# Performance work log

Hardware: AMD Instinct MI355X
Metric: run time of the kernel (lower is better)

The kernel has to match this reference:

```python
import jax, jax.numpy as jnp
import numpy as np

N, M, D, H = 16, 1024, 64, 4  # batch, num_node, dim_in==dim_hid, num_head
NEG_SLOPE = 0.2


def setup_inputs() -> dict:
    key = jax.random.key(0)
    ks = jax.random.split(key, 10)
    s = 1.0 / np.sqrt(D)
    inp = {
        "x": jax.random.normal(ks[0], (N, M, D), dtype=jnp.float32),
        "edge": jnp.zeros((N, M, M), dtype=jnp.float32),  # unused by the module
        # stacked per-head Linear(dim_in, dim_hid) params: weight (H, D_out, D_in), bias (H, D_out)
        "Wk": (jax.random.normal(ks[1], (H, D, D), dtype=jnp.float32) * s),
        "bk": (jax.random.normal(ks[2], (H, D), dtype=jnp.float32) * s),
        "Wq": (jax.random.normal(ks[3], (H, D, D), dtype=jnp.float32) * s),
        "bq": (jax.random.normal(ks[4], (H, D), dtype=jnp.float32) * s),
        "Wv": (jax.random.normal(ks[5], (H, D, D), dtype=jnp.float32) * s),
        "bv": (jax.random.normal(ks[6], (H, D), dtype=jnp.float32) * s),
        # decoder: Linear(dim_hid*num_head -> dim_in)
        "Wdec": (jax.random.normal(ks[7], (D, H * D), dtype=jnp.float32) / np.sqrt(H * D)),
        "bdec": (jax.random.normal(ks[8], (D,), dtype=jnp.float32) / np.sqrt(H * D)),
    }
    return inp


def reference(x, edge, Wk, bk, Wq, bq, Wv, bv, Wdec, bdec):
    # x: (N, M, D). Per head h: K = x @ Wk[h].T + bk[h], etc.
    K = jnp.einsum("nmd,hed->nhme", x, Wk) + bk[None, :, None, :]  # (N,H,M,D)
    Q = jnp.einsum("nmd,hed->nhme", x, Wq) + bq[None, :, None, :]
    V = jnp.einsum("nmd,hed->nhme", x, Wv) + bv[None, :, None, :]
    # alpha[n,h,i,j] = K[n,h,i] . Q[n,h,j]  (sender=K row i, receiver=Q row j)
    alpha = jnp.einsum("nhie,nhje->nhij", K, Q)  # (N,H,M,M)
    alpha = jax.nn.leaky_relu(alpha, NEG_SLOPE)
    alpha = jax.nn.softmax(alpha, axis=-1)
    agg = jnp.einsum("nhij,nhje->nhie", alpha, V)  # (N,H,M,D)
    dx = jax.nn.leaky_relu(agg, NEG_SLOPE) - x[:, None, :, :]  # (N,H,M,D)
    # concat heads along feature dim (head 0 first): (N, M, H*D)
    dx = dx.transpose(0, 2, 1, 3).reshape(N, M, H * D)
    return dx @ Wdec.T + bdec  # (N, M, D)
```

## Files before the change

### kernel.cpp

```cpp
#include <hip/hip_runtime.h>
#include <hip/hip_bf16.h>


#define NB 16
#define MM 1024
#define DD 64
#define HH 4
#define NEG 0.2f
#define AST 72
#define DST 264

typedef __attribute__((ext_vector_type(8))) short bf16x8;
typedef __attribute__((ext_vector_type(8))) _Float16 f16x8;
typedef __attribute__((ext_vector_type(16))) float f32x16;

__device__ inline unsigned short f2bf(float f) {
  unsigned int u = __builtin_bit_cast(unsigned int, f);
  return (unsigned short)((u + 0x7FFFu + ((u >> 16) & 1u)) >> 16);
}
__device__ inline unsigned short f2h(float f) {
  _Float16 h = (_Float16)f;
  return __builtin_bit_cast(unsigned short, h);
}
__device__ inline unsigned int pack_bf16(float a, float b) {
  unsigned int ua = __builtin_bit_cast(unsigned int, a);
  unsigned int ub = __builtin_bit_cast(unsigned int, b);
  ua = (ua + 0x7FFFu + ((ua >> 16) & 1u)) >> 16;
  ub = (ub + 0x7FFFu + ((ub >> 16) & 1u)) & 0xFFFF0000u;
  return ua | ub;
}

__global__ __launch_bounds__(256) void proj_kernel(
    const float* __restrict__ x,
    const float* __restrict__ Wk, const float* __restrict__ Wq, const float* __restrict__ Wv,
    const float* __restrict__ bk, const float* __restrict__ bq, const float* __restrict__ bv,
    unsigned short* __restrict__ Kf, unsigned short* __restrict__ Qf,
    unsigned short* __restrict__ Vtg) {
  __shared__ unsigned short xs[64 * AST];
  __shared__ unsigned short ob[64 * AST];
  const int t = threadIdx.x;
  const int r0 = blockIdx.x * 64;
  const int combo = blockIdx.y, mat = combo >> 2, h = combo & 3;
  const int n = r0 >> 10, ml = r0 & 1023;
  const float* W = mat == 0 ? Wk : (mat == 1 ? Wq : Wv);
  const float* bias = mat == 0 ? bk : (mat == 1 ? bq : bv);

#pragma unroll
  for (int rep = 0; rep < 2; ++rep) {
    int idx = rep * 256 + t, row = idx >> 3, c8 = (idx & 7) * 8;
    float4 a = *(const float4*)&x[(size_t)(r0 + row) * DD + c8];
    float4 b = *(const float4*)&x[(size_t)(r0 + row) * DD + c8 + 4];
    unsigned short p[8] = {f2h(a.x), f2h(a.y), f2h(a.z), f2h(a.w),
                           f2h(b.x), f2h(b.y), f2h(b.z), f2h(b.w)};
    *(uint4*)&xs[row * AST + c8] = *(uint4*)p;
  }
  __syncthreads();

  const int w = t >> 6, lane = t & 63, m31 = lane & 31, hf = lane >> 5;
  const int mi = w >> 1, ne = w & 1;
  const int ecol = h * 64 + ne * 32 + m31;
  const float bb = bias[ecol];

  f32x16 C;
#pragma unroll
  for (int r = 0; r < 16; ++r) C[r] = 0.f;
#pragma unroll
  for (int ks = 0; ks < 4; ++ks) {
    f16x8 xa = *(f16x8*)&xs[(mi * 32 + m31) * AST + ks * 16 + hf * 8];
    float4 wa = *(const float4*)&W[(size_t)ecol * DD + ks * 16 + hf * 8];
    float4 wc = *(const float4*)&W[(size_t)ecol * DD + ks * 16 + hf * 8 + 4];
    f16x8 wb;
    wb[0] = (_Float16)wa.x; wb[1] = (_Float16)wa.y; wb[2] = (_Float16)wa.z; wb[3] = (_Float16)wa.w;
    wb[4] = (_Float16)wc.x; wb[5] = (_Float16)wc.y; wb[6] = (_Float16)wc.z; wb[7] = (_Float16)wc.w;
    C = __builtin_amdgcn_mfma_f32_32x32x16_f16(xa, wb, C, 0, 0, 0);
  }

  if (mat < 2) {
#pragma unroll
    for (int r = 0; r < 16; ++r) {
      int rr = (r & 3) + 8 * (r >> 2) + 4 * hf;
      ob[(mi * 32 + rr) * AST + ne * 32 + m31] = f2h(C[r] + bb);
    }
  } else {
#pragma unroll
    for (int r = 0; r < 16; ++r) {
      int rr = (r & 3) + 8 * (r >> 2) + 4 * hf;
      ob[(ne * 32 + m31) * AST + mi * 32 + rr] = f2bf(C[r] + bb);
    }
  }
  __syncthreads();

  if (mat < 2) {
    unsigned short* dst = mat == 0 ? Kf : Qf;
    const size_t obase = (((size_t)n * HH + h) * MM + ml) * DD;
#pragma unroll
    for (int rep = 0; rep < 2; ++rep) {
      int idx = rep * 256 + t, row = idx >> 3, c8 = (idx & 7) * 8;
      *(uint4*)&dst[obase + (size_t)row * DD + c8] = *(uint4*)&ob[row * AST + c8];
    }
  } else {
    const size_t obase = (((size_t)n * HH + h) * DD) * MM + ml;
#pragma unroll
    for (int rep = 0; rep < 2; ++rep) {
      int idx = rep * 256 + t, row = idx >> 3, c8 = (idx & 7) * 8;
      *(uint4*)&Vtg[obase + (size_t)row * MM + c8] = *(uint4*)&ob[row * AST + c8];
    }
  }
}

__global__ __launch_bounds__(256, 4) void attn_kernel(
    const unsigned short* __restrict__ Kf, const unsigned short* __restrict__ Qf,
    const unsigned short* __restrict__ Vtg, const float* __restrict__ x,
    unsigned short* __restrict__ DX) {
  __shared__ unsigned short smem[2 * 64 * AST];
  __shared__ float lsp[2][64];
  unsigned short* qh = smem;
  unsigned short* vt = smem + 64 * AST;

  const int t = threadIdx.x;
  const int w = t >> 6, lane = t & 63, m31 = lane & 31, hf = lane >> 5;
  const int ih = w >> 1, jh = w & 1;
  const int i0 = blockIdx.x * 64, h = blockIdx.y, n = blockIdx.z;
  const size_t base = (((size_t)n * HH + h) * MM) * DD;
  const size_t baseT = (((size_t)n * HH + h) * DD) * MM;
  const int irow = i0 + ih * 32 + m31;

  f16x8 kf[4];
#pragma unroll
  for (int ks = 0; ks < 4; ++ks)
    kf[ks] = *(const f16x8*)&Kf[base + (size_t)irow * DD + ks * 16 + hf * 8];

  f32x16 agg0, agg1;
#pragma unroll
  for (int r = 0; r < 16; ++r) { agg0[r] = 0.f; agg1[r] = 0.f; }
  float lsum = 0.f;

  for (int jt = 0; jt < 16; ++jt) {
    const int j0 = jt * 64;
    __syncthreads();
#pragma unroll
    for (int rep = 0; rep < 2; ++rep) {
      int idx = rep * 256 + t, row = idx >> 3, c8 = (idx & 7) * 8;
      *(uint4*)&qh[row * AST + c8] = *(const uint4*)&Qf[base + (size_t)(j0 + row) * DD + c8];
      *(uint4*)&vt[row * AST + c8] = *(const uint4*)&Vtg[baseT + (size_t)row * MM + j0 + c8];
    }
    __syncthreads();

    f32x16 C;
#pragma unroll
    for (int r = 0; r < 16; ++r) C[r] = 0.f;
#pragma unroll
    for (int ks = 0; ks < 4; ++ks) {
      f16x8 qa = *(f16x8*)&qh[(jh * 32 + m31) * AST + ks * 16 + hf * 8];
      C = __builtin_amdgcn_mfma_f32_32x32x16_f16(qa, kf[ks], C, 0, 0, 0);
    }
    unsigned int pk[8];
#pragma unroll
    for (int g = 0; g < 4; ++g) {
      float p0 = C[4 * g + 0], p1 = C[4 * g + 1], p2 = C[4 * g + 2], p3 = C[4 * g + 3];
      p0 = __expf(fmaxf(p0, NEG * p0));
      p1 = __expf(fmaxf(p1, NEG * p1));
      p2 = __expf(fmaxf(p2, NEG * p2));
      p3 = __expf(fmaxf(p3, NEG * p3));
      lsum += (p0 + p1) + (p2 + p3);
      pk[g * 2]     = pack_bf16(p0, p1);
      pk[g * 2 + 1] = pack_bf16(p2, p3);
    }

#pragma unroll
    for (int kk = 0; kk < 2; ++kk) {
      const int gl2 = kk * 4, gh2 = kk * 4 + 2;
      unsigned int sA = hf ? pk[gl2]     : pk[gh2];
      unsigned int sB = hf ? pk[gl2 + 1] : pk[gh2 + 1];
      unsigned int rA = (unsigned int)__shfl_xor((int)sA, 32);
      unsigned int rB = (unsigned int)__shfl_xor((int)sB, 32);
      union { unsigned int u[4]; bf16x8 v; } cv;
      cv.u[0] = hf ? rA : pk[gl2];
      cv.u[1] = hf ? rB : pk[gl2 + 1];
      cv.u[2] = hf ? pk[gh2]     : rA;
      cv.u[3] = hf ? pk[gh2 + 1] : rB;
      bf16x8 bV0 = *(bf16x8*)&vt[m31 * AST + jh * 32 + kk * 16 + hf * 8];
      bf16x8 bV1 = *(bf16x8*)&vt[(32 + m31) * AST + jh * 32 + kk * 16 + hf * 8];
      agg0 = __builtin_amdgcn_mfma_f32_32x32x16_bf16(cv.v, bV0, agg0, 0, 0, 0);
      agg1 = __builtin_amdgcn_mfma_f32_32x32x16_bf16(cv.v, bV1, agg1, 0, 0, 0);
    }
  }

  lsum += __shfl_xor(lsum, 32);
  __syncthreads();
  if (hf == 0) lsp[jh][ih * 32 + m31] = lsum;
  float* red = (float*)smem;
  const int slot = ih * 2304 + m31 * 72 + hf * 36;
  if (jh == 1) {
#pragma unroll
    for (int c = 0; c < 4; ++c) {
      *(float4*)&red[slot + 4 * c]      = make_float4(agg0[4*c], agg0[4*c+1], agg0[4*c+2], agg0[4*c+3]);
      *(float4*)&red[slot + 16 + 4 * c] = make_float4(agg1[4*c], agg1[4*c+1], agg1[4*c+2], agg1[4*c+3]);
    }
  }
  __syncthreads();
  if (jh == 0) {
#pragma unroll
    for (int c = 0; c < 4; ++c) {
      float4 v0 = *(float4*)&red[slot + 4 * c];
      float4 v1 = *(float4*)&red[slot + 16 + 4 * c];
      agg0[4*c] += v0.x; agg0[4*c+1] += v0.y; agg0[4*c+2] += v0.z; agg0[4*c+3] += v0.w;
      agg1[4*c] += v1.x; agg1[4*c+1] += v1.y; agg1[4*c+2] += v1.z; agg1[4*c+3] += v1.w;
    }
    float invl[16];
#pragma unroll
    for (int r = 0; r < 16; ++r) {
      int rr = (r & 3) + 8 * (r >> 2) + 4 * hf;
      invl[r] = 1.0f / (lsp[0][ih * 32 + rr] + lsp[1][ih * 32 + rr]);
    }
#pragma unroll
    for (int r = 0; r < 16; ++r) {
      int rr = (r & 3) + 8 * (r >> 2) + 4 * hf;
      const size_t row = (size_t)n * MM + i0 + ih * 32 + rr;
      float v0 = agg0[r] * invl[r];
      v0 = fmaxf(v0, NEG * v0);
      v0 -= x[row * DD + m31];
      DX[row * (HH * DD) + h * DD + m31] = f2h(v0);
      float v1 = agg1[r] * invl[r];
      v1 = fmaxf(v1, NEG * v1);
      v1 -= x[row * DD + 32 + m31];
      DX[row * (HH * DD) + h * DD + 32 + m31] = f2h(v1);
    }
  }
}

__global__ __launch_bounds__(256) void dec_kernel(
    const unsigned short* __restrict__ DX, const float* __restrict__ Wdec,
    const float* __restrict__ bdec, float* __restrict__ out) {
  __shared__ unsigned short dxs[32 * DST];
  __shared__ float red2[2 * 64 * 20];
  const int t = threadIdx.x;
  const int w = t >> 6, lane = t & 63, m31 = lane & 31, hf = lane >> 5;
  const int nd = w & 1, kq = w >> 1;
  const int r0 = blockIdx.x * 32;
#pragma unroll
  for (int rep = 0; rep < 4; ++rep) {
    int idx = rep * 256 + t, row = idx >> 5, c8 = (idx & 31) * 8;
    *(uint4*)&dxs[row * DST + c8] = *(const uint4*)&DX[(size_t)(r0 + row) * 256 + c8];
  }
  __syncthreads();
  f32x16 C;
#pragma unroll
  for (int r = 0; r < 16; ++r) C[r] = 0.f;
#pragma unroll
  for (int ks = 0; ks < 8; ++ks) {
    const int koff = kq * 128 + ks * 16 + hf * 8;
    f16x8 aD = *(f16x8*)&dxs[m31 * DST + koff];
    float4 wa = *(const float4*)&Wdec[(size_t)(nd * 32 + m31) * 256 + koff];
    float4 wc = *(const float4*)&Wdec[(size_t)(nd * 32 + m31) * 256 + koff + 4];
    f16x8 bW;
    bW[0] = (_Float16)wa.x; bW[1] = (_Float16)wa.y; bW[2] = (_Float16)wa.z; bW[3] = (_Float16)wa.w;
    bW[4] = (_Float16)wc.x; bW[5] = (_Float16)wc.y; bW[6] = (_Float16)wc.z; bW[7] = (_Float16)wc.w;
    C = __builtin_amdgcn_mfma_f32_32x32x16_f16(aD, bW, C, 0, 0, 0);
  }
  const int slot = nd * 64 * 20 + (hf * 32 + m31) * 20;
  if (kq == 1) {
#pragma unroll
    for (int c = 0; c < 4; ++c)
      *(float4*)&red2[slot + 4 * c] = make_float4(C[4*c], C[4*c+1], C[4*c+2], C[4*c+3]);
  }
  __syncthreads();
  if (kq == 0) {
#pragma unroll
    for (int c = 0; c < 4; ++c) {
      float4 v = *(float4*)&red2[slot + 4 * c];
      C[4*c] += v.x; C[4*c+1] += v.y; C[4*c+2] += v.z; C[4*c+3] += v.w;
    }
    const float bb = bdec[nd * 32 + m31];
#pragma unroll
    for (int r = 0; r < 16; ++r) {
      int rr = (r & 3) + 8 * (r >> 2) + 4 * hf;
      out[(size_t)(r0 + rr) * DD + nd * 32 + m31] = C[r] + bb;
    }
  }
}

extern "C" void kernel_launch(void* const* d_in, const int* in_sizes, int n_in,
                              void* d_out, int out_size, void* d_ws, size_t ws_size,
                              hipStream_t stream) {
  const float* x    = (const float*)d_in[0];
  const float* Wk   = (const float*)d_in[2];
  const float* bk   = (const float*)d_in[3];
  const float* Wq   = (const float*)d_in[4];
  const float* bq   = (const float*)d_in[5];
  const float* Wv   = (const float*)d_in[6];
  const float* bv   = (const float*)d_in[7];
  const float* Wdec = (const float*)d_in[8];
  const float* bdec = (const float*)d_in[9];
  float* out = (float*)d_out;

  const size_t seg = (size_t)NB * HH * MM * DD;
  unsigned short* Kf  = (unsigned short*)d_ws;
  unsigned short* Qf  = Kf + seg;
  unsigned short* Vt  = Qf + seg;
  unsigned short* DXp = Vt + seg;

  proj_kernel<<<dim3(256, 12), 256, 0, stream>>>(x, Wk, Wq, Wv, bk, bq, bv, Kf, Qf, Vt);
  attn_kernel<<<dim3(16, HH, NB), 256, 0, stream>>>(Kf, Qf, Vt, x, DXp);
  dec_kernel<<<NB * MM / 32, 256, 0, stream>>>(DXp, Wdec, bdec, out);
}
```

Before: 166.6 us.

## Fuse K/Q/V projections, prefetch attention tiles, use exp2, and simplify decoder

The projection kernel now computes K, Q and V for one head per block, so each block stages x once instead of three times, and it also converts Wdec to fp16 into the workspace. The K projection is pre-scaled by log2(e) so the attention softmax can use the hardware exp2 directly. The attention loop register-prefetches the next Q/V tile while the current one is computed. bf16 packing of probabilities now truncates instead of rounding. The decoder drops LDS staging and the split-K reduction, running 128-thread blocks that read DX and the fp16 Wdec directly from global memory. The trade-offs are slightly lower precision from truncation, more registers per attention thread, and fewer, heavier projection blocks.

```diff
diff --git a/kernel.cpp b/kernel.cpp
--- a/kernel.cpp
+++ b/kernel.cpp
@@ -7,8 +7,8 @@
 #define DD 64
 #define HH 4
 #define NEG 0.2f
+#define L2E 1.44269504f
 #define AST 72
-#define DST 264
 
 typedef __attribute__((ext_vector_type(8))) short bf16x8;
 typedef __attribute__((ext_vector_type(8))) _Float16 f16x8;
@@ -22,28 +22,40 @@
   _Float16 h = (_Float16)f;
   return __builtin_bit_cast(unsigned short, h);
 }
-__device__ inline unsigned int pack_bf16(float a, float b) {
+__device__ inline unsigned int pack_bf16_tr(float a, float b) {
   unsigned int ua = __builtin_bit_cast(unsigned int, a);
   unsigned int ub = __builtin_bit_cast(unsigned int, b);
-  ua = (ua + 0x7FFFu + ((ua >> 16) & 1u)) >> 16;
-  ub = (ub + 0x7FFFu + ((ub >> 16) & 1u)) & 0xFFFF0000u;
-  return ua | ub;
+  return (ua >> 16) | (ub & 0xFFFF0000u);
+}
+__device__ inline f16x8 cvtW8(const float* p) {
+  float4 a = *(const float4*)p;
+  float4 b = *(const float4*)(p + 4);
+  f16x8 r;
+  r[0] = (_Float16)a.x; r[1] = (_Float16)a.y; r[2] = (_Float16)a.z; r[3] = (_Float16)a.w;
+  r[4] = (_Float16)b.x; r[5] = (_Float16)b.y; r[6] = (_Float16)b.z; r[7] = (_Float16)b.w;
+  return r;
 }
 
 __global__ __launch_bounds__(256) void proj_kernel(
     const float* __restrict__ x,
     const float* __restrict__ Wk, const float* __restrict__ Wq, const float* __restrict__ Wv,
     const float* __restrict__ bk, const float* __restrict__ bq, const float* __restrict__ bv,
+    const float* __restrict__ Wdec,
     unsigned short* __restrict__ Kf, unsigned short* __restrict__ Qf,
-    unsigned short* __restrict__ Vtg) {
+    unsigned short* __restrict__ Vtg, unsigned short* __restrict__ Wdf) {
   __shared__ unsigned short xs[64 * AST];
   __shared__ unsigned short ob[64 * AST];
   const int t = threadIdx.x;
   const int r0 = blockIdx.x * 64;
-  const int combo = blockIdx.y, mat = combo >> 2, h = combo & 3;
+  const int h = blockIdx.y;
   const int n = r0 >> 10, ml = r0 & 1023;
-  const float* W = mat == 0 ? Wk : (mat == 1 ? Wq : Wv);
-  const float* bias = mat == 0 ? bk : (mat == 1 ? bq : bv);
+
+  if (h == 0 && blockIdx.x < 16) {
+    int idx = (blockIdx.x * 256 + t) * 4;
+    float4 v = *(const float4*)&Wdec[idx];
+    unsigned short p[4] = {f2h(v.x), f2h(v.y), f2h(v.z), f2h(v.w)};
+    *(uint2*)&Wdf[idx] = *(uint2*)p;
+  }
 
 #pragma unroll
   for (int rep = 0; rep < 2; ++rep) {
@@ -59,52 +71,59 @@
   const int w = t >> 6, lane = t & 63, m31 = lane & 31, hf = lane >> 5;
   const int mi = w >> 1, ne = w & 1;
   const int ecol = h * 64 + ne * 32 + m31;
-  const float bb = bias[ecol];
-
-  f32x16 C;
-#pragma unroll
-  for (int r = 0; r < 16; ++r) C[r] = 0.f;
+
+  f32x16 Ck, Cq, Cv;
+#pragma unroll
+  for (int r = 0; r < 16; ++r) { Ck[r] = 0.f; Cq[r] = 0.f; Cv[r] = 0.f; }
 #pragma unroll
   for (int ks = 0; ks < 4; ++ks) {
     f16x8 xa = *(f16x8*)&xs[(mi * 32 + m31) * AST + ks * 16 + hf * 8];
-    float4 wa = *(const float4*)&W[(size_t)ecol * DD + ks * 16 + hf * 8];
-    float4 wc = *(const float4*)&W[(size_t)ecol * DD + ks * 16 + hf * 8 + 4];
-    f16x8 wb;
-    wb[0] = (_Float16)wa.x; wb[1] = (_Float16)wa.y; wb[2] = (_Float16)wa.z; wb[3] = (_Float16)wa.w;
-    wb[4] = (_Float16)wc.x; wb[5] = (_Float16)wc.y; wb[6] = (_Float16)wc.z; wb[7] = (_Float16)wc.w;
-    C = __builtin_amdgcn_mfma_f32_32x32x16_f16(xa, wb, C, 0, 0, 0);
-  }
-
-  if (mat < 2) {
-#pragma unroll
-    for (int r = 0; r < 16; ++r) {
-      int rr = (r & 3) + 8 * (r >> 2) + 4 * hf;
-      ob[(mi * 32 + rr) * AST + ne * 32 + m31] = f2h(C[r] + bb);
-    }
-  } else {
-#pragma unroll
-    for (int r = 0; r < 16; ++r) {
-      int rr = (r & 3) + 8 * (r >> 2) + 4 * hf;
-      ob[(ne * 32 + m31) * AST + mi * 32 + rr] = f2bf(C[r] + bb);
-    }
-  }
-  __syncthreads();
-
-  if (mat < 2) {
-    unsigned short* dst = mat == 0 ? Kf : Qf;
-    const size_t obase = (((size_t)n * HH + h) * MM + ml) * DD;
-#pragma unroll
-    for (int rep = 0; rep < 2; ++rep) {
-      int idx = rep * 256 + t, row = idx >> 3, c8 = (idx & 7) * 8;
-      *(uint4*)&dst[obase + (size_t)row * DD + c8] = *(uint4*)&ob[row * AST + c8];
-    }
-  } else {
-    const size_t obase = (((size_t)n * HH + h) * DD) * MM + ml;
-#pragma unroll
-    for (int rep = 0; rep < 2; ++rep) {
-      int idx = rep * 256 + t, row = idx >> 3, c8 = (idx & 7) * 8;
-      *(uint4*)&Vtg[obase + (size_t)row * MM + c8] = *(uint4*)&ob[row * AST + c8];
-    }
+    f16x8 wk8 = cvtW8(&Wk[(size_t)ecol * DD + ks * 16 + hf * 8]);
+    Ck = __builtin_amdgcn_mfma_f32_32x32x16_f16(xa, wk8, Ck, 0, 0, 0);
+    f16x8 wq8 = cvtW8(&Wq[(size_t)ecol * DD + ks * 16 + hf * 8]);
+    Cq = __builtin_amdgcn_mfma_f32_32x32x16_f16(xa, wq8, Cq, 0, 0, 0);
+    f16x8 wv8 = cvtW8(&Wv[(size_t)ecol * DD + ks * 16 + hf * 8]);
+    Cv = __builtin_amdgcn_mfma_f32_32x32x16_f16(xa, wv8, Cv, 0, 0, 0);
+  }
+  const float bbk = bk[ecol], bbq = bq[ecol], bbv = bv[ecol];
+
+  const size_t obase = (((size_t)n * HH + h) * MM + ml) * DD;
+  const size_t obaseT = (((size_t)n * HH + h) * DD) * MM + ml;
+
+#pragma unroll
+  for (int r = 0; r < 16; ++r) {
+    int rr = (r & 3) + 8 * (r >> 2) + 4 * hf;
+    ob[(mi * 32 + rr) * AST + ne * 32 + m31] = f2h((Ck[r] + bbk) * L2E);
+  }
+  __syncthreads();
+#pragma unroll
+  for (int rep = 0; rep < 2; ++rep) {
+    int idx = rep * 256 + t, row = idx >> 3, c8 = (idx & 7) * 8;
+    *(uint4*)&Kf[obase + (size_t)row * DD + c8] = *(uint4*)&ob[row * AST + c8];
+  }
+  __syncthreads();
+#pragma unroll
+  for (int r = 0; r < 16; ++r) {
+    int rr = (r & 3) + 8 * (r >> 2) + 4 * hf;
+    ob[(mi * 32 + rr) * AST + ne * 32 + m31] = f2h(Cq[r] + bbq);
+  }
+  __syncthreads();
+#pragma unroll
+  for (int rep = 0; rep < 2; ++rep) {
+    int idx = rep * 256 + t, row = idx >> 3, c8 = (idx & 7) * 8;
+    *(uint4*)&Qf[obase + (size_t)row * DD + c8] = *(uint4*)&ob[row * AST + c8];
+  }
+  __syncthreads();
+#pragma unroll
+  for (int r = 0; r < 16; ++r) {
+    int rr = (r & 3) + 8 * (r >> 2) + 4 * hf;
+    ob[(ne * 32 + m31) * AST + mi * 32 + rr] = f2bf(Cv[r] + bbv);
+  }
+  __syncthreads();
+#pragma unroll
+  for (int rep = 0; rep < 2; ++rep) {
+    int idx = rep * 256 + t, row = idx >> 3, c8 = (idx & 7) * 8;
+    *(uint4*)&Vtg[obaseT + (size_t)row * MM + c8] = *(uint4*)&ob[row * AST + c8];
   }
 }
 
@@ -124,6 +143,7 @@
   const size_t base = (((size_t)n * HH + h) * MM) * DD;
   const size_t baseT = (((size_t)n * HH + h) * DD) * MM;
   const int irow = i0 + ih * 32 + m31;
+  const int srow0 = t >> 3, srow1 = srow0 + 32, c8 = (t & 7) * 8;
 
   f16x8 kf[4];
 #pragma unroll
@@ -135,16 +155,25 @@
   for (int r = 0; r < 16; ++r) { agg0[r] = 0.f; agg1[r] = 0.f; }
   float lsum = 0.f;
 
+  uint4 rq0 = *(const uint4*)&Qf[base + (size_t)srow0 * DD + c8];
+  uint4 rq1 = *(const uint4*)&Qf[base + (size_t)srow1 * DD + c8];
+  uint4 rv0 = *(const uint4*)&Vtg[baseT + (size_t)srow0 * MM + c8];
+  uint4 rv1 = *(const uint4*)&Vtg[baseT + (size_t)srow1 * MM + c8];
+
   for (int jt = 0; jt < 16; ++jt) {
-    const int j0 = jt * 64;
     __syncthreads();
-#pragma unroll
-    for (int rep = 0; rep < 2; ++rep) {
-      int idx = rep * 256 + t, row = idx >> 3, c8 = (idx & 7) * 8;
-      *(uint4*)&qh[row * AST + c8] = *(const uint4*)&Qf[base + (size_t)(j0 + row) * DD + c8];
-      *(uint4*)&vt[row * AST + c8] = *(const uint4*)&Vtg[baseT + (size_t)row * MM + j0 + c8];
-    }
+    *(uint4*)&qh[srow0 * AST + c8] = rq0;
+    *(uint4*)&qh[srow1 * AST + c8] = rq1;
+    *(uint4*)&vt[srow0 * AST + c8] = rv0;
+    *(uint4*)&vt[srow1 * AST + c8] = rv1;
     __syncthreads();
+    if (jt < 15) {
+      const int j1 = (jt + 1) * 64;
+      rq0 = *(const uint4*)&Qf[base + (size_t)(j1 + srow0) * DD + c8];
+      rq1 = *(const uint4*)&Qf[base + (size_t)(j1 + srow1) * DD + c8];
+      rv0 = *(const uint4*)&Vtg[baseT + (size_t)srow0 * MM + j1 + c8];
+      rv1 = *(const uint4*)&Vtg[baseT + (size_t)srow1 * MM + j1 + c8];
+    }
 
     f32x16 C;
 #pragma unroll
@@ -158,13 +187,13 @@
 #pragma unroll
     for (int g = 0; g < 4; ++g) {
       float p0 = C[4 * g + 0], p1 = C[4 * g + 1], p2 = C[4 * g + 2], p3 = C[4 * g + 3];
-      p0 = __expf(fmaxf(p0, NEG * p0));
-      p1 = __expf(fmaxf(p1, NEG * p1));
-      p2 = __expf(fmaxf(p2, NEG * p2));
-      p3 = __expf(fmaxf(p3, NEG * p3));
+      p0 = __builtin_amdgcn_exp2f(fmaxf(p0, NEG * p0));
+      p1 = __builtin_amdgcn_exp2f(fmaxf(p1, NEG * p1));
+      p2 = __builtin_amdgcn_exp2f(fmaxf(p2, NEG * p2));
+      p3 = __builtin_amdgcn_exp2f(fmaxf(p3, NEG * p3));
       lsum += (p0 + p1) + (p2 + p3);
-      pk[g * 2]     = pack_bf16(p0, p1);
-      pk[g * 2 + 1] = pack_bf16(p2, p3);
+      pk[g * 2]     = pack_bf16_tr(p0, p1);
+      pk[g * 2 + 1] = pack_bf16_tr(p2, p3);
     }
 
 #pragma unroll
@@ -229,54 +258,26 @@
   }
 }
 
-__global__ __launch_bounds__(256) void dec_kernel(
-    const unsigned short* __restrict__ DX, const float* __restrict__ Wdec,
+__global__ __launch_bounds__(128) void dec_kernel(
+    const unsigned short* __restrict__ DX, const unsigned short* __restrict__ Wdf,
     const float* __restrict__ bdec, float* __restrict__ out) {
-  __shared__ unsigned short dxs[32 * DST];
-  __shared__ float red2[2 * 64 * 20];
   const int t = threadIdx.x;
-  const int w = t >> 6, lane = t & 63, m31 = lane & 31, hf = lane >> 5;
-  const int nd = w & 1, kq = w >> 1;
+  const int nd = t >> 6, lane = t & 63, m31 = lane & 31, hf = lane >> 5;
   const int r0 = blockIdx.x * 32;
-#pragma unroll
-  for (int rep = 0; rep < 4; ++rep) {
-    int idx = rep * 256 + t, row = idx >> 5, c8 = (idx & 31) * 8;
-    *(uint4*)&dxs[row * DST + c8] = *(const uint4*)&DX[(size_t)(r0 + row) * 256 + c8];
-  }
-  __syncthreads();
   f32x16 C;
 #pragma unroll
   for (int r = 0; r < 16; ++r) C[r] = 0.f;
 #pragma unroll
-  for (int ks = 0; ks < 8; ++ks) {
-    const int koff = kq * 128 + ks * 16 + hf * 8;
-    f16x8 aD = *(f16x8*)&dxs[m31 * DST + koff];
-    float4 wa = *(const float4*)&Wdec[(size_t)(nd * 32 + m31) * 256 + koff];
-    float4 wc = *(const float4*)&Wdec[(size_t)(nd * 32 + m31) * 256 + koff + 4];
-    f16x8 bW;
-    bW[0] = (_Float16)wa.x; bW[1] = (_Float16)wa.y; bW[2] = (_Float16)wa.z; bW[3] = (_Float16)wa.w;
-    bW[4] = (_Float16)wc.x; bW[5] = (_Float16)wc.y; bW[6] = (_Float16)wc.z; bW[7] = (_Float16)wc.w;
+  for (int ks = 0; ks < 16; ++ks) {
+    f16x8 aD = *(const f16x8*)&DX[(size_t)(r0 + m31) * 256 + ks * 16 + hf * 8];
+    f16x8 bW = *(const f16x8*)&Wdf[(size_t)(nd * 32 + m31) * 256 + ks * 16 + hf * 8];
     C = __builtin_amdgcn_mfma_f32_32x32x16_f16(aD, bW, C, 0, 0, 0);
   }
-  const int slot = nd * 64 * 20 + (hf * 32 + m31) * 20;
-  if (kq == 1) {
-#pragma unroll
-    for (int c = 0; c < 4; ++c)
-      *(float4*)&red2[slot + 4 * c] = make_float4(C[4*c], C[4*c+1], C[4*c+2], C[4*c+3]);
-  }
-  __syncthreads();
-  if (kq == 0) {
-#pragma unroll
-    for (int c = 0; c < 4; ++c) {
-      float4 v = *(float4*)&red2[slot + 4 * c];
-      C[4*c] += v.x; C[4*c+1] += v.y; C[4*c+2] += v.z; C[4*c+3] += v.w;
-    }
-    const float bb = bdec[nd * 32 + m31];
-#pragma unroll
-    for (int r = 0; r < 16; ++r) {
-      int rr = (r & 3) + 8 * (r >> 2) + 4 * hf;
-      out[(size_t)(r0 + rr) * DD + nd * 32 + m31] = C[r] + bb;
-    }
+  const float bb = bdec[nd * 32 + m31];
+#pragma unroll
+  for (int r = 0; r < 16; ++r) {
+    int rr = (r & 3) + 8 * (r >> 2) + 4 * hf;
+    out[(size_t)(r0 + rr) * DD + nd * 32 + m31] = C[r] + bb;
   }
 }
 
@@ -299,8 +300,10 @@
   unsigned short* Qf  = Kf + seg;
   unsigned short* Vt  = Qf + seg;
   unsigned short* DXp = Vt + seg;
-
-  proj_kernel<<<dim3(256, 12), 256, 0, stream>>>(x, Wk, Wq, Wv, bk, bq, bv, Kf, Qf, Vt);
+  unsigned short* Wdf = DXp + seg;
+
+  proj_kernel<<<dim3(256, HH), 256, 0, stream>>>(x, Wk, Wq, Wv, bk, bq, bv, Wdec,
+                                                 Kf, Qf, Vt, Wdf);
   attn_kernel<<<dim3(16, HH, NB), 256, 0, stream>>>(Kf, Qf, Vt, x, DXp);
-  dec_kernel<<<NB * MM / 32, 256, 0, stream>>>(DXp, Wdec, bdec, out);
-}
+  dec_kernel<<<NB * MM / 32, 128, 0, stream>>>(DXp, Wdf, bdec, out);
+}
```

Measured after the change: 162.2 us. 1.03x faster.
